# Kernel optimization log

Measured on AMD Instinct MI355X. Metric: run time of the kernel, lower is better.

The kernel has to match this reference:

```python
import jax, jax.numpy as jnp
import numpy as np

B, S, NX, H = 8, 1024, 1024, 16
D = NX // H  # head dim = 64


def setup_inputs() -> dict:
    key = jax.random.key(0)
    k1, k2, k3 = jax.random.split(key, 3)
    x = jax.random.normal(k1, (B, S, NX), dtype=jnp.float32)
    Wqkv = jax.random.normal(k2, (NX, 3 * NX), dtype=jnp.float32) * 0.02
    bqkv = jnp.zeros((3 * NX,), dtype=jnp.float32)
    Wproj = jax.random.normal(k3, (NX, NX), dtype=jnp.float32) * 0.02
    bproj = jnp.zeros((NX,), dtype=jnp.float32)
    return {"x": x, "Wqkv": Wqkv, "bqkv": bqkv, "Wproj": Wproj, "bproj": bproj}


def reference(x, Wqkv, bqkv, Wproj, bproj):
    # c_attn: Conv1D == x @ W + b
    qkv = jnp.einsum('bsn,nm->bsm', x, Wqkv) + bqkv  # [B,S,3*NX]
    q, k, v = jnp.split(qkv, 3, axis=-1)
    # split heads -> [B,H,S,D]
    def split_heads(t):
        return t.reshape(B, S, H, D).transpose(0, 2, 1, 3)
    q, k, v = split_heads(q), split_heads(k), split_heads(v)
    # present = stack(key, value) with key as [B,H,S,D]
    present = jnp.stack((k, v))  # [2,B,H,S,D]
    # scores, scaled (scale=True) by sqrt(head_dim)
    w = jnp.einsum('bhqd,bhkd->bhqk', q, k) / jnp.sqrt(jnp.asarray(D, x.dtype))
    bias = jnp.tril(jnp.ones((S, S), dtype=x.dtype))[None, None]  # causal tril buffer
    w = w * bias - 10000.0 * (1.0 - bias)
    w = jax.nn.softmax(w, axis=-1)
    a = jnp.einsum('bhqk,bhkd->bhqd', w, v)  # [B,H,S,D]
    a = a.transpose(0, 2, 1, 3).reshape(B, S, NX)  # merge heads
    a = jnp.einsum('bsn,nm->bsm', a, Wproj) + bproj  # c_proj
    return a, present
```

## Files before the change

### kernel.cpp

```cpp
#include <hip/hip_runtime.h>
#include <stdint.h>


#define BB 8
#define SS 1024
#define NXX 1024
#define NH 16
#define HD 64

typedef __bf16 bf16x8 __attribute__((ext_vector_type(8)));
typedef float  floatx4 __attribute__((ext_vector_type(4)));
typedef unsigned short ushort8 __attribute__((ext_vector_type(8)));
typedef unsigned short ushortx4 __attribute__((ext_vector_type(4)));

__device__ inline float bf2f(unsigned short u) {
    unsigned int x = ((unsigned int)u) << 16;
    float f;
    __builtin_memcpy(&f, &x, 4);
    return f;
}
__device__ inline unsigned short f2bf(float f) {
    unsigned int u;
    __builtin_memcpy(&u, &f, 4);
    u += 0x7FFFu + ((u >> 16) & 1u);
    return (unsigned short)(u >> 16);
}

__device__ inline void gload_lds16(const unsigned short* g, unsigned short* l) {
    __builtin_amdgcn_global_load_lds(
        (const __attribute__((address_space(1))) void*)g,
        (__attribute__((address_space(3))) void*)l, 16, 0, 0);
}

__global__ void sniff_k(const unsigned short* __restrict__ x, int* __restrict__ flag) {
    if (threadIdx.x == 0 && blockIdx.x == 0) {
        int g = 0;
        for (int i = 0; i < 512; i++) {
            float f = bf2f(x[i]);
            float a = fabsf(f);
            if (!(a <= 1e4f)) g++;
            else if (f != 0.f && a < 1e-35f) g++;
        }
        *flag = (g > 16) ? 1 : 0;
    }
}

__global__ __launch_bounds__(256) void prep(
    const void* __restrict__ x, const void* __restrict__ Wqkv,
    const void* __restrict__ Wproj,
    unsigned short* __restrict__ xbf, unsigned short* __restrict__ WqkvT,
    unsigned short* __restrict__ WprojT, const int* __restrict__ flagp) {
    const int f32 = *flagp;
    int blk = blockIdx.x;
    if (blk < 4096) {
        const size_t i = ((size_t)blk * 256 + threadIdx.x) * 8;
        if (f32) {
            const floatx4* p = (const floatx4*)((const float*)x + i);
            floatx4 f0 = p[0], f1 = p[1];
            ushort8 u;
#pragma unroll
            for (int j = 0; j < 4; j++) { u[j] = f2bf(f0[j]); u[4 + j] = f2bf(f1[j]); }
            *(ushort8*)(xbf + i) = u;
        } else {
            *(ushort8*)(xbf + i) = *(const ushort8*)((const unsigned short*)x + i);
        }
        return;
    }
    blk -= 4096;
    const void* in;
    unsigned short* out;
    int R, C;
    if (blk < 3072) { in = Wqkv; out = WqkvT; R = 1024; C = 3072; }
    else            { blk -= 3072; in = Wproj; out = WprojT; R = 1024; C = 1024; }
    const int ctiles = C / 32;
    const int c0 = (blk % ctiles) * 32, r0 = (blk / ctiles) * 32;

    __shared__ unsigned short tile[32][33];
    const int tx = threadIdx.x & 31, ty = threadIdx.x >> 5;
    if (f32) {
        const float* inf = (const float*)in;
#pragma unroll
        for (int i = ty; i < 32; i += 8)
            tile[i][tx] = f2bf(inf[(size_t)(r0 + i) * C + c0 + tx]);
    } else {
        const unsigned short* inu = (const unsigned short*)in;
#pragma unroll
        for (int i = ty; i < 32; i += 8)
            tile[i][tx] = inu[(size_t)(r0 + i) * C + c0 + tx];
    }
    __syncthreads();
#pragma unroll
    for (int i = ty; i < 32; i += 8)
        out[(size_t)(c0 + i) * R + r0 + tx] = tile[tx][i];
}

__global__ __launch_bounds__(256) void transpose_v(
    const void* __restrict__ outbase, unsigned short* __restrict__ vbfT,
    const int* __restrict__ flagp) {
    const int f32 = *flagp;
    const int blk = blockIdx.x;
    const int sb = blk & 15;
    const int bh = blk >> 4;
    const int tid = threadIdx.x;
    const int r = tid >> 2;
    const int c0 = (tid & 3) * 16;
    __shared__ unsigned short tile[64][72];
    const int perm = ((r & 15) << 2) | (r >> 4);
    const size_t esz = f32 ? 4 : 2;
    const char* vbase = (const char*)outbase + (size_t)(2 * BB * SS * NXX) * esz;
    if (f32) {
        const float* src = (const float*)vbase + ((size_t)bh * SS + sb * 64 + r) * HD + c0;
#pragma unroll
        for (int j = 0; j < 16; j++) tile[c0 + j][perm] = f2bf(src[j]);
    } else {
        const unsigned short* src = (const unsigned short*)vbase + ((size_t)bh * SS + sb * 64 + r) * HD + c0;
#pragma unroll
        for (int j = 0; j < 16; j++) tile[c0 + j][perm] = src[j];
    }
    __syncthreads();
    const int d = tid >> 2;
    const int o0 = (tid & 3) * 16;
    unsigned short* dst = vbfT + ((size_t)(bh * HD + d)) * SS + sb * 64 + o0;
    *(ushort8*)dst       = *(const ushort8*)&tile[d][o0];
    *(ushort8*)(dst + 8) = *(const ushort8*)&tile[d][o0 + 8];
}

template <int MODE>
__global__ __launch_bounds__(256) void gemm_bt(
    const unsigned short* __restrict__ A,
    const unsigned short* __restrict__ Bt,
    const void* __restrict__ bias,
    void* __restrict__ outbase,
    unsigned short* __restrict__ q_ws,
    unsigned short* __restrict__ kbf,
    int M, int N, int K, const int* __restrict__ flagp) {
    __shared__ __align__(16) unsigned short As[128 * 32];
    __shared__ __align__(16) unsigned short Bs[128 * 32];

    const int f32 = *flagp;
    const int tid  = threadIdx.x;
    const int lane = tid & 63;
    const int wave = tid >> 6;
    const int wr = wave >> 1, wc = wave & 1;
    const int l15 = lane & 15;
    const int quad = lane >> 4;
    const int row0 = blockIdx.y * 128;
    const int col0 = blockIdx.x * 128;

    floatx4 acc[4][4];
    floatx4 zz = {0.f, 0.f, 0.f, 0.f};
#pragma unroll
    for (int i = 0; i < 4; i++)
#pragma unroll
        for (int j = 0; j < 4; j++) acc[i][j] = zz;

    const int lrow = lane >> 2;
    const int lcol = (lane & 3) * 8;
    const unsigned short* Ag = A  + (size_t)(row0 + wave * 32 + lrow) * K + lcol;
    const unsigned short* Bg = Bt + (size_t)(col0 + wave * 32 + lrow) * K + lcol;
    unsigned short* Asl0 = &As[(wave * 32) * 32];
    unsigned short* Asl1 = &As[(wave * 32 + 16) * 32];
    unsigned short* Bsl0 = &Bs[(wave * 32) * 32];
    unsigned short* Bsl1 = &Bs[(wave * 32 + 16) * 32];

    for (int k0 = 0; k0 < K; k0 += 32) {
        gload_lds16(Ag + k0, Asl0);
        gload_lds16(Ag + k0 + (size_t)16 * K, Asl1);
        gload_lds16(Bg + k0, Bsl0);
        gload_lds16(Bg + k0 + (size_t)16 * K, Bsl1);
        __syncthreads();

        bf16x8 af[4], bfr[4];
#pragma unroll
        for (int mi = 0; mi < 4; mi++)
            af[mi] = *(const bf16x8*)&As[(wr * 64 + mi * 16 + l15) * 32 + quad * 8];
#pragma unroll
        for (int ni = 0; ni < 4; ni++)
            bfr[ni] = *(const bf16x8*)&Bs[(wc * 64 + ni * 16 + l15) * 32 + quad * 8];
#pragma unroll
        for (int mi = 0; mi < 4; mi++)
#pragma unroll
            for (int ni = 0; ni < 4; ni++)
                acc[mi][ni] = __builtin_amdgcn_mfma_f32_16x16x32_bf16(af[mi], bfr[ni], acc[mi][ni], 0, 0, 0);
        __syncthreads();
    }

    float bv[4];
#pragma unroll
    for (int ni = 0; ni < 4; ni++) {
        const int colb = col0 + wc * 64 + ni * 16 + l15;
        bv[ni] = f32 ? ((const float*)bias)[colb] : bf2f(((const unsigned short*)bias)[colb]);
    }

    if (MODE == 0) {
#pragma unroll
        for (int mi = 0; mi < 4; mi++)
#pragma unroll
            for (int ni = 0; ni < 4; ni++) {
                const int colb = col0 + wc * 64 + ni * 16 + l15;
#pragma unroll
                for (int i = 0; i < 4; i++) {
                    const int row = row0 + wr * 64 + mi * 16 + quad * 4 + i;
                    const float val = acc[mi][ni][i] + bv[ni];
                    const size_t idx = (size_t)row * N + colb;
                    if (f32) ((float*)outbase)[idx] = val;
                    else     ((unsigned short*)outbase)[idx] = f2bf(val);
                }
            }
        return;
    }

    const int sec = col0 >> 10;
    const size_t esz = f32 ? 4 : 2;
    const int b = row0 >> 10;
    const int s0 = row0 & 1023;

    if (sec == 0) {
#pragma unroll
        for (int mi = 0; mi < 4; mi++)
#pragma unroll
            for (int ni = 0; ni < 4; ni++) {
                const int colb = col0 + wc * 64 + ni * 16 + l15;
                const int h = (colb & 1023) >> 6, d = colb & 63;
#pragma unroll
                for (int i = 0; i < 4; i++) {
                    const int s = s0 + wr * 64 + mi * 16 + quad * 4 + i;
                    q_ws[(size_t)((b * NH + h) * SS + s) * HD + d] = f2bf(acc[mi][ni][i] + bv[ni]);
                }
            }
    } else if (sec == 1) {
        char* kbase = (char*)outbase + (size_t)(BB * SS * NXX) * esz;
#pragma unroll
        for (int mi = 0; mi < 4; mi++)
#pragma unroll
            for (int ni = 0; ni < 4; ni++) {
                const int colb = col0 + wc * 64 + ni * 16 + l15;
                const int h = (colb & 1023) >> 6, d = colb & 63;
#pragma unroll
                for (int i = 0; i < 4; i++) {
                    const int s = s0 + wr * 64 + mi * 16 + quad * 4 + i;
                    const float val = acc[mi][ni][i] + bv[ni];
                    const size_t idx = (size_t)((b * NH + h) * SS + s) * HD + d;
                    if (f32) ((float*)kbase)[idx] = val;
                    else     ((unsigned short*)kbase)[idx] = f2bf(val);
                    kbf[idx] = f2bf(val);
                }
            }
    } else {
        char* vbase = (char*)outbase + (size_t)(2 * BB * SS * NXX) * esz;
#pragma unroll
        for (int mi = 0; mi < 4; mi++)
#pragma unroll
            for (int ni = 0; ni < 4; ni++) {
                const int colb = col0 + wc * 64 + ni * 16 + l15;
                const int h = (colb & 1023) >> 6, d = colb & 63;
#pragma unroll
                for (int i = 0; i < 4; i++) {
                    const int s = s0 + wr * 64 + mi * 16 + quad * 4 + i;
                    const float val = acc[mi][ni][i] + bv[ni];
                    const size_t idx = (size_t)((b * NH + h) * SS + s) * HD + d;
                    if (f32) ((float*)vbase)[idx] = val;
                    else     ((unsigned short*)vbase)[idx] = f2bf(val);
                }
            }
    }
}

__global__ __launch_bounds__(256) void attn(
    const unsigned short* __restrict__ q_ws,
    const unsigned short* __restrict__ kbf,
    const unsigned short* __restrict__ vbfT,
    unsigned short* __restrict__ amerged) {
    const int tid = threadIdx.x;
    const int lane = tid & 63;
    const int w = tid >> 6;
    const int l15 = lane & 15, quad = lane >> 4;
    const int blk = blockIdx.x;
    const int p = blk & 3;
    const int bh = blk >> 2;
    const int b = bh >> 4, h = bh & 15;

    const unsigned short* Q = q_ws + (size_t)bh * (SS * HD);
    const unsigned short* K = kbf + (size_t)bh * (SS * HD);
    const unsigned short* V = vbfT + (size_t)bh * (HD * SS);

    __shared__ __align__(16) unsigned short Ks[64][72];
    __shared__ __align__(16) unsigned short Vs[64][72];
    __shared__ __align__(16) unsigned short Pl[4][32][72];

    floatx4 zz = {0.f, 0.f, 0.f, 0.f};
    ushort8 ones_u;
#pragma unroll
    for (int j = 0; j < 8; j++) ones_u[j] = 0x3F80;
    const bf16x8 ones = __builtin_bit_cast(bf16x8, ones_u);

    const int srow = tid >> 2;
    const int soff = (tid & 3) * 16;

#pragma unroll
    for (int tile = 0; tile < 2; tile++) {
        const int qb = tile ? (7 - p) : p;
        const int qbase = qb * 128;
        const int wrow0 = qbase + w * 32;
        const int wq_max = wrow0 + 31;
        const int jend = qbase + 128;

        bf16x8 qa[2][2];
#pragma unroll
        for (int m = 0; m < 2; m++)
#pragma unroll
            for (int t = 0; t < 2; t++)
                qa[m][t] = *(const bf16x8*)&Q[(size_t)(wrow0 + m * 16 + l15) * HD + t * 32 + quad * 8];

        floatx4 o[2][4], o5[2];
        float mrow[2][4];
#pragma unroll
        for (int m = 0; m < 2; m++) {
            o5[m] = zz;
#pragma unroll
            for (int i = 0; i < 4; i++) mrow[m][i] = -1e30f;
#pragma unroll
            for (int nf = 0; nf < 4; nf++) o[m][nf] = zz;
        }

        *(ushort8*)&Ks[srow][soff]     = *(const ushort8*)&K[(size_t)srow * HD + soff];
        *(ushort8*)&Ks[srow][soff + 8] = *(const ushort8*)&K[(size_t)srow * HD + soff + 8];
        *(ushort8*)&Vs[srow][soff]     = *(const ushort8*)&V[(size_t)srow * SS + soff];
        *(ushort8*)&Vs[srow][soff + 8] = *(const ushort8*)&V[(size_t)srow * SS + soff + 8];
        __syncthreads();

        for (int j0 = 0; j0 < jend; j0 += 64) {
            const bool havenext = (j0 + 64 < jend);
            ushort8 kn0, kn1, vn0, vn1;
            if (havenext) {
                kn0 = *(const ushort8*)&K[(size_t)(j0 + 64 + srow) * HD + soff];
                kn1 = *(const ushort8*)&K[(size_t)(j0 + 64 + srow) * HD + soff + 8];
                vn0 = *(const ushort8*)&V[(size_t)srow * SS + j0 + 64 + soff];
                vn1 = *(const ushort8*)&V[(size_t)srow * SS + j0 + 64 + soff + 8];
            }

            if (j0 <= wq_max) {
                floatx4 sf[2][4];
#pragma unroll
                for (int kg = 0; kg < 4; kg++) {
                    bf16x8 kb0 = *(const bf16x8*)&Ks[kg * 16 + l15][quad * 8];
                    bf16x8 kb1 = *(const bf16x8*)&Ks[kg * 16 + l15][32 + quad * 8];
#pragma unroll
                    for (int m = 0; m < 2; m++) {
                        floatx4 s = zz;
                        s = __builtin_amdgcn_mfma_f32_16x16x32_bf16(qa[m][0], kb0, s, 0, 0, 0);
                        s = __builtin_amdgcn_mfma_f32_16x16x32_bf16(qa[m][1], kb1, s, 0, 0, 0);
                        sf[m][kg] = s;
                    }
                }

                float alpha_[2][4];
#pragma unroll
                for (int m = 0; m < 2; m++)
#pragma unroll
                    for (int i = 0; i < 4; i++) {
                        const int qrow = wrow0 + m * 16 + quad * 4 + i;
                        float pv4[4];
#pragma unroll
                        for (int kg = 0; kg < 4; kg++) {
                            const int key = j0 + kg * 16 + l15;
                            float s = sf[m][kg][i] * 0.125f;
                            if (key > qrow) s = -10000.0f;
                            pv4[kg] = s;
                        }
                        float t = fmaxf(fmaxf(pv4[0], pv4[1]), fmaxf(pv4[2], pv4[3]));
                        t = fmaxf(t, __shfl_xor(t, 1));
                        t = fmaxf(t, __shfl_xor(t, 2));
                        t = fmaxf(t, __shfl_xor(t, 4));
                        t = fmaxf(t, __shfl_xor(t, 8));
                        const float mnew = fmaxf(mrow[m][i], t);
                        alpha_[m][i] = __expf(mrow[m][i] - mnew);
                        mrow[m][i] = mnew;
                        ushortx4 pk;
#pragma unroll
                        for (int kg = 0; kg < 4; kg++)
                            pk[kg] = f2bf(__expf(pv4[kg] - mnew));
                        *(ushortx4*)&Pl[w][m * 16 + quad * 4 + i][l15 * 4] = pk;
                    }

#pragma unroll
                for (int m = 0; m < 2; m++) {
#pragma unroll
                    for (int i = 0; i < 4; i++) o5[m][i] *= alpha_[m][i];
#pragma unroll
                    for (int nf = 0; nf < 4; nf++)
#pragma unroll
                        for (int i = 0; i < 4; i++) o[m][nf][i] *= alpha_[m][i];
                }

                bf16x8 pa[2][2];
#pragma unroll
                for (int m = 0; m < 2; m++) {
                    pa[m][0] = *(const bf16x8*)&Pl[w][m * 16 + l15][quad * 8];
                    pa[m][1] = *(const bf16x8*)&Pl[w][m * 16 + l15][32 + quad * 8];
                }

#pragma unroll
                for (int m = 0; m < 2; m++) {
                    o5[m] = __builtin_amdgcn_mfma_f32_16x16x32_bf16(pa[m][0], ones, o5[m], 0, 0, 0);
                    o5[m] = __builtin_amdgcn_mfma_f32_16x16x32_bf16(pa[m][1], ones, o5[m], 0, 0, 0);
                }
#pragma unroll
                for (int nf = 0; nf < 4; nf++) {
                    bf16x8 vb0 = *(const bf16x8*)&Vs[nf * 16 + l15][quad * 8];
                    bf16x8 vb1 = *(const bf16x8*)&Vs[nf * 16 + l15][32 + quad * 8];
#pragma unroll
                    for (int m = 0; m < 2; m++) {
                        o[m][nf] = __builtin_amdgcn_mfma_f32_16x16x32_bf16(pa[m][0], vb0, o[m][nf], 0, 0, 0);
                        o[m][nf] = __builtin_amdgcn_mfma_f32_16x16x32_bf16(pa[m][1], vb1, o[m][nf], 0, 0, 0);
                    }
                }
            }
            __syncthreads();
            if (havenext) {
                *(ushort8*)&Ks[srow][soff]     = kn0;
                *(ushort8*)&Ks[srow][soff + 8] = kn1;
                *(ushort8*)&Vs[srow][soff]     = vn0;
                *(ushort8*)&Vs[srow][soff + 8] = vn1;
            }
            __syncthreads();
        }

#pragma unroll
        for (int m = 0; m < 2; m++)
#pragma unroll
            for (int nf = 0; nf < 4; nf++)
#pragma unroll
                for (int i = 0; i < 4; i++) {
                    const int s = wrow0 + m * 16 + quad * 4 + i;
                    amerged[(size_t)(b * SS + s) * NXX + h * HD + nf * 16 + l15] =
                        f2bf(o[m][nf][i] / o5[m][i]);
                }
        __syncthreads();
    }
}

extern "C" void kernel_launch(void* const* d_in, const int* in_sizes, int n_in,
                              void* d_out, int out_size, void* d_ws, size_t ws_size,
                              hipStream_t stream) {
    const void* x     = d_in[0];
    const void* Wqkv  = d_in[1];
    const void* bqkv  = d_in[2];
    const void* Wproj = d_in[3];
    const void* bproj = d_in[4];

    int* flag = (int*)d_ws;
    unsigned short* ws = (unsigned short*)d_ws + 8;
    unsigned short* WqkvT   = ws;
    unsigned short* WprojT  = WqkvT + 3072 * 1024;
    unsigned short* q_ws    = WprojT + 1024 * 1024;
    unsigned short* kbf     = q_ws + 8 * 1024 * 1024;
    unsigned short* vbfT    = kbf + 8 * 1024 * 1024;
    unsigned short* amerged = vbfT + 8 * 1024 * 1024;
    unsigned short* xbf     = amerged;

    sniff_k<<<1, 64, 0, stream>>>((const unsigned short*)x, flag);
    prep<<<dim3(8192), 256, 0, stream>>>(x, Wqkv, Wproj, xbf, WqkvT, WprojT, flag);
    gemm_bt<1><<<dim3(3072 / 128, 8192 / 128), 256, 0, stream>>>(
        xbf, WqkvT, bqkv, d_out, q_ws, kbf, 8192, 3072, 1024, flag);
    transpose_v<<<dim3(128 * 16), 256, 0, stream>>>(d_out, vbfT, flag);
    attn<<<dim3(BB * NH * 4), 256, 0, stream>>>(q_ws, kbf, vbfT, amerged);
    gemm_bt<0><<<dim3(1024 / 128, 8192 / 128), 256, 0, stream>>>(
        amerged, WprojT, bproj, d_out, nullptr, nullptr, 8192, 1024, 1024, flag);
}
```

Before: 374.7 us.

## Double-buffer GEMM LDS tiles and read attention K/V directly from global

The GEMM kernel now double-buffers its A/B shared-memory tiles and issues the next tile's global-to-LDS loads before computing on the current one, so each k-step needs one barrier instead of two. The attention kernel drops the shared K/V staging and its block-wide barriers. Each wave now loads its K and V fragments straight from global memory and runs only up to its own causal limit. This removes sync stalls and lets waves proceed independently, at the cost of redundant per-wave global/L2 reads of K and V. It also relies on an explicit lgkmcnt wait to order the per-wave P-tile writes before they are read back.

New measurement: 390.6 us. 4.3% more time.

```diff
diff --git a/kernel.cpp b/kernel.cpp
--- a/kernel.cpp
+++ b/kernel.cpp
@@ -134,8 +134,8 @@
     unsigned short* __restrict__ q_ws,
     unsigned short* __restrict__ kbf,
     int M, int N, int K, const int* __restrict__ flagp) {
-    __shared__ __align__(16) unsigned short As[128 * 32];
-    __shared__ __align__(16) unsigned short Bs[128 * 32];
+    __shared__ __align__(16) unsigned short As[2][128 * 32];
+    __shared__ __align__(16) unsigned short Bs[2][128 * 32];
 
     const int f32 = *flagp;
     const int tid  = threadIdx.x;
@@ -158,31 +158,41 @@
     const int lcol = (lane & 3) * 8;
     const unsigned short* Ag = A  + (size_t)(row0 + wave * 32 + lrow) * K + lcol;
     const unsigned short* Bg = Bt + (size_t)(col0 + wave * 32 + lrow) * K + lcol;
-    unsigned short* Asl0 = &As[(wave * 32) * 32];
-    unsigned short* Asl1 = &As[(wave * 32 + 16) * 32];
-    unsigned short* Bsl0 = &Bs[(wave * 32) * 32];
-    unsigned short* Bsl1 = &Bs[(wave * 32 + 16) * 32];
-
+    const int sl0 = (wave * 32) * 32;
+    const int sl1 = (wave * 32 + 16) * 32;
+
+    gload_lds16(Ag, &As[0][sl0]);
+    gload_lds16(Ag + (size_t)16 * K, &As[0][sl1]);
+    gload_lds16(Bg, &Bs[0][sl0]);
+    gload_lds16(Bg + (size_t)16 * K, &Bs[0][sl1]);
+    __syncthreads();
+
+    int cur = 0;
     for (int k0 = 0; k0 < K; k0 += 32) {
-        gload_lds16(Ag + k0, Asl0);
-        gload_lds16(Ag + k0 + (size_t)16 * K, Asl1);
-        gload_lds16(Bg + k0, Bsl0);
-        gload_lds16(Bg + k0 + (size_t)16 * K, Bsl1);
-        __syncthreads();
+        if (k0 + 32 < K) {
+            const unsigned short* Agn = Ag + k0 + 32;
+            const unsigned short* Bgn = Bg + k0 + 32;
+            gload_lds16(Agn, &As[cur ^ 1][sl0]);
+            gload_lds16(Agn + (size_t)16 * K, &As[cur ^ 1][sl1]);
+            gload_lds16(Bgn, &Bs[cur ^ 1][sl0]);
+            gload_lds16(Bgn + (size_t)16 * K, &Bs[cur ^ 1][sl1]);
+        }
 
         bf16x8 af[4], bfr[4];
 #pragma unroll
         for (int mi = 0; mi < 4; mi++)
-            af[mi] = *(const bf16x8*)&As[(wr * 64 + mi * 16 + l15) * 32 + quad * 8];
+            af[mi] = *(const bf16x8*)&As[cur][(wr * 64 + mi * 16 + l15) * 32 + quad * 8];
 #pragma unroll
         for (int ni = 0; ni < 4; ni++)
-            bfr[ni] = *(const bf16x8*)&Bs[(wc * 64 + ni * 16 + l15) * 32 + quad * 8];
+            bfr[ni] = *(const bf16x8*)&Bs[cur][(wc * 64 + ni * 16 + l15) * 32 + quad * 8];
 #pragma unroll
         for (int mi = 0; mi < 4; mi++)
 #pragma unroll
             for (int ni = 0; ni < 4; ni++)
                 acc[mi][ni] = __builtin_amdgcn_mfma_f32_16x16x32_bf16(af[mi], bfr[ni], acc[mi][ni], 0, 0, 0);
+
         __syncthreads();
+        cur ^= 1;
     }
 
     float bv[4];
@@ -284,8 +294,6 @@
     const unsigned short* K = kbf + (size_t)bh * (SS * HD);
     const unsigned short* V = vbfT + (size_t)bh * (HD * SS);
 
-    __shared__ __align__(16) unsigned short Ks[64][72];
-    __shared__ __align__(16) unsigned short Vs[64][72];
     __shared__ __align__(16) unsigned short Pl[4][32][72];
 
     floatx4 zz = {0.f, 0.f, 0.f, 0.f};
@@ -294,16 +302,11 @@
     for (int j = 0; j < 8; j++) ones_u[j] = 0x3F80;
     const bf16x8 ones = __builtin_bit_cast(bf16x8, ones_u);
 
-    const int srow = tid >> 2;
-    const int soff = (tid & 3) * 16;
-
 #pragma unroll
     for (int tile = 0; tile < 2; tile++) {
         const int qb = tile ? (7 - p) : p;
-        const int qbase = qb * 128;
-        const int wrow0 = qbase + w * 32;
+        const int wrow0 = qb * 128 + w * 32;
         const int wq_max = wrow0 + 31;
-        const int jend = qbase + 128;
 
         bf16x8 qa[2][2];
 #pragma unroll
@@ -323,107 +326,87 @@
             for (int nf = 0; nf < 4; nf++) o[m][nf] = zz;
         }
 
-        *(ushort8*)&Ks[srow][soff]     = *(const ushort8*)&K[(size_t)srow * HD + soff];
-        *(ushort8*)&Ks[srow][soff + 8] = *(const ushort8*)&K[(size_t)srow * HD + soff + 8];
-        *(ushort8*)&Vs[srow][soff]     = *(const ushort8*)&V[(size_t)srow * SS + soff];
-        *(ushort8*)&Vs[srow][soff + 8] = *(const ushort8*)&V[(size_t)srow * SS + soff + 8];
-        __syncthreads();
-
-        for (int j0 = 0; j0 < jend; j0 += 64) {
-            const bool havenext = (j0 + 64 < jend);
-            ushort8 kn0, kn1, vn0, vn1;
-            if (havenext) {
-                kn0 = *(const ushort8*)&K[(size_t)(j0 + 64 + srow) * HD + soff];
-                kn1 = *(const ushort8*)&K[(size_t)(j0 + 64 + srow) * HD + soff + 8];
-                vn0 = *(const ushort8*)&V[(size_t)srow * SS + j0 + 64 + soff];
-                vn1 = *(const ushort8*)&V[(size_t)srow * SS + j0 + 64 + soff + 8];
-            }
-
-            if (j0 <= wq_max) {
-                floatx4 sf[2][4];
-#pragma unroll
-                for (int kg = 0; kg < 4; kg++) {
-                    bf16x8 kb0 = *(const bf16x8*)&Ks[kg * 16 + l15][quad * 8];
-                    bf16x8 kb1 = *(const bf16x8*)&Ks[kg * 16 + l15][32 + quad * 8];
-#pragma unroll
-                    for (int m = 0; m < 2; m++) {
-                        floatx4 s = zz;
-                        s = __builtin_amdgcn_mfma_f32_16x16x32_bf16(qa[m][0], kb0, s, 0, 0, 0);
-                        s = __builtin_amdgcn_mfma_f32_16x16x32_bf16(qa[m][1], kb1, s, 0, 0, 0);
-                        sf[m][kg] = s;
+        for (int j0 = 0; j0 <= wq_max; j0 += 64) {
+            floatx4 sf[2][4];
+#pragma unroll
+            for (int kg = 0; kg < 4; kg++) {
+                const size_t krow = (size_t)(j0 + kg * 16 + l15) * HD;
+                bf16x8 kb0 = *(const bf16x8*)&K[krow + quad * 8];
+                bf16x8 kb1 = *(const bf16x8*)&K[krow + 32 + quad * 8];
+#pragma unroll
+                for (int m = 0; m < 2; m++) {
+                    floatx4 s = zz;
+                    s = __builtin_amdgcn_mfma_f32_16x16x32_bf16(qa[m][0], kb0, s, 0, 0, 0);
+                    s = __builtin_amdgcn_mfma_f32_16x16x32_bf16(qa[m][1], kb1, s, 0, 0, 0);
+                    sf[m][kg] = s;
+                }
+            }
+
+            float alpha_[2][4];
+#pragma unroll
+            for (int m = 0; m < 2; m++)
+#pragma unroll
+                for (int i = 0; i < 4; i++) {
+                    const int qrow = wrow0 + m * 16 + quad * 4 + i;
+                    float pv4[4];
+#pragma unroll
+                    for (int kg = 0; kg < 4; kg++) {
+                        const int key = j0 + kg * 16 + l15;
+                        float s = sf[m][kg][i] * 0.125f;
+                        if (key > qrow) s = -10000.0f;
+                        pv4[kg] = s;
                     }
-                }
-
-                float alpha_[2][4];
-#pragma unroll
-                for (int m = 0; m < 2; m++)
-#pragma unroll
-                    for (int i = 0; i < 4; i++) {
-                        const int qrow = wrow0 + m * 16 + quad * 4 + i;
-                        float pv4[4];
-#pragma unroll
-                        for (int kg = 0; kg < 4; kg++) {
-                            const int key = j0 + kg * 16 + l15;
-                            float s = sf[m][kg][i] * 0.125f;
-                            if (key > qrow) s = -10000.0f;
-                            pv4[kg] = s;
-                        }
-                        float t = fmaxf(fmaxf(pv4[0], pv4[1]), fmaxf(pv4[2], pv4[3]));
-                        t = fmaxf(t, __shfl_xor(t, 1));
-                        t = fmaxf(t, __shfl_xor(t, 2));
-                        t = fmaxf(t, __shfl_xor(t, 4));
-                        t = fmaxf(t, __shfl_xor(t, 8));
-                        const float mnew = fmaxf(mrow[m][i], t);
-                        alpha_[m][i] = __expf(mrow[m][i] - mnew);
-                        mrow[m][i] = mnew;
-                        ushortx4 pk;
-#pragma unroll
-                        for (int kg = 0; kg < 4; kg++)
-                            pk[kg] = f2bf(__expf(pv4[kg] - mnew));
-                        *(ushortx4*)&Pl[w][m * 16 + quad * 4 + i][l15 * 4] = pk;
-                    }
-
+                    float t = fmaxf(fmaxf(pv4[0], pv4[1]), fmaxf(pv4[2], pv4[3]));
+                    t = fmaxf(t, __shfl_xor(t, 1));
+                    t = fmaxf(t, __shfl_xor(t, 2));
+                    t = fmaxf(t, __shfl_xor(t, 4));
+                    t = fmaxf(t, __shfl_xor(t, 8));
+                    const float mnew = fmaxf(mrow[m][i], t);
+                    alpha_[m][i] = __expf(mrow[m][i] - mnew);
+                    mrow[m][i] = mnew;
+                    ushortx4 pk;
+#pragma unroll
+                    for (int kg = 0; kg < 4; kg++)
+                        pk[kg] = f2bf(__expf(pv4[kg] - mnew));
+                    *(ushortx4*)&Pl[w][m * 16 + quad * 4 + i][l15 * 4] = pk;
+                }
+
+#pragma unroll
+            for (int m = 0; m < 2; m++) {
+#pragma unroll
+                for (int i = 0; i < 4; i++) o5[m][i] *= alpha_[m][i];
+#pragma unroll
+                for (int nf = 0; nf < 4; nf++)
+#pragma unroll
+                    for (int i = 0; i < 4; i++) o[m][nf][i] *= alpha_[m][i];
+            }
+
+            asm volatile("s_waitcnt lgkmcnt(0)" ::: "memory");
+            __builtin_amdgcn_sched_barrier(0);
+
+            bf16x8 pa[2][2];
+#pragma unroll
+            for (int m = 0; m < 2; m++) {
+                pa[m][0] = *(const bf16x8*)&Pl[w][m * 16 + l15][quad * 8];
+                pa[m][1] = *(const bf16x8*)&Pl[w][m * 16 + l15][32 + quad * 8];
+            }
+
+#pragma unroll
+            for (int m = 0; m < 2; m++) {
+                o5[m] = __builtin_amdgcn_mfma_f32_16x16x32_bf16(pa[m][0], ones, o5[m], 0, 0, 0);
+                o5[m] = __builtin_amdgcn_mfma_f32_16x16x32_bf16(pa[m][1], ones, o5[m], 0, 0, 0);
+            }
+#pragma unroll
+            for (int nf = 0; nf < 4; nf++) {
+                const size_t vrow = (size_t)(nf * 16 + l15) * SS + j0;
+                bf16x8 vb0 = *(const bf16x8*)&V[vrow + quad * 8];
+                bf16x8 vb1 = *(const bf16x8*)&V[vrow + 32 + quad * 8];
 #pragma unroll
                 for (int m = 0; m < 2; m++) {
-#pragma unroll
-                    for (int i = 0; i < 4; i++) o5[m][i] *= alpha_[m][i];
-#pragma unroll
-                    for (int nf = 0; nf < 4; nf++)
-#pragma unroll
-                        for (int i = 0; i < 4; i++) o[m][nf][i] *= alpha_[m][i];
-                }
-
-                bf16x8 pa[2][2];
-#pragma unroll
-                for (int m = 0; m < 2; m++) {
-                    pa[m][0] = *(const bf16x8*)&Pl[w][m * 16 + l15][quad * 8];
-                    pa[m][1] = *(const bf16x8*)&Pl[w][m * 16 + l15][32 + quad * 8];
-                }
-
-#pragma unroll
-                for (int m = 0; m < 2; m++) {
-                    o5[m] = __builtin_amdgcn_mfma_f32_16x16x32_bf16(pa[m][0], ones, o5[m], 0, 0, 0);
-                    o5[m] = __builtin_amdgcn_mfma_f32_16x16x32_bf16(pa[m][1], ones, o5[m], 0, 0, 0);
-                }
-#pragma unroll
-                for (int nf = 0; nf < 4; nf++) {
-                    bf16x8 vb0 = *(const bf16x8*)&Vs[nf * 16 + l15][quad * 8];
-                    bf16x8 vb1 = *(const bf16x8*)&Vs[nf * 16 + l15][32 + quad * 8];
-#pragma unroll
-                    for (int m = 0; m < 2; m++) {
-                        o[m][nf] = __builtin_amdgcn_mfma_f32_16x16x32_bf16(pa[m][0], vb0, o[m][nf], 0, 0, 0);
-                        o[m][nf] = __builtin_amdgcn_mfma_f32_16x16x32_bf16(pa[m][1], vb1, o[m][nf], 0, 0, 0);
-                    }
-                }
-            }
-            __syncthreads();
-            if (havenext) {
-                *(ushort8*)&Ks[srow][soff]     = kn0;
-                *(ushort8*)&Ks[srow][soff + 8] = kn1;
-                *(ushort8*)&Vs[srow][soff]     = vn0;
-                *(ushort8*)&Vs[srow][soff + 8] = vn1;
-            }
-            __syncthreads();
+                    o[m][nf] = __builtin_amdgcn_mfma_f32_16x16x32_bf16(pa[m][0], vb0, o[m][nf], 0, 0, 0);
+                    o[m][nf] = __builtin_amdgcn_mfma_f32_16x16x32_bf16(pa[m][1], vb1, o[m][nf], 0, 0, 0);
+                }
+            }
         }
 
 #pragma unroll
@@ -436,7 +419,6 @@
                     amerged[(size_t)(b * SS + s) * NXX + h * HD + nf * 16 + l15] =
                         f2bf(o[m][nf][i] / o5[m][i]);
                 }
-        __syncthreads();
     }
 }
 
```

## Rewrite GEMMs as 256x256-tile 8-wave kernels with double-buffered pipelined loads

Applied to the files above, without the earlier changes.

Replaces the 128x128, 4-wave GEMM with a 256x256-tile, 8-wave kernel. It double-buffers A and B in LDS with XOR-swizzled layout and K-step 64, and issues the next tiles' global-to-LDS loads in phases between MFMA bursts, using raw barriers, vmcnt waits and setprio. Block IDs are remapped to group tiles for locality. The aim is to hide global load latency, raise data reuse per tile and cut LDS bank conflicts. In exchange it needs far more registers and LDS (128KB) and leaves fewer blocks, e.g. 128 for the projection GEMM, which may underfill the 256 CUs.

Measured after the change: 346.7 us. -7.4%, faster.

```diff
diff --git a/kernel.cpp b/kernel.cpp
--- a/kernel.cpp
+++ b/kernel.cpp
@@ -7,6 +7,8 @@
 #define NXX 1024
 #define NH 16
 #define HD 64
+#define KK 1024
+#define NKT 16
 
 typedef __bf16 bf16x8 __attribute__((ext_vector_type(8)));
 typedef float  floatx4 __attribute__((ext_vector_type(4)));
@@ -31,6 +33,16 @@
         (const __attribute__((address_space(1))) void*)g,
         (__attribute__((address_space(3))) void*)l, 16, 0, 0);
 }
+
+__device__ inline void barrier_raw() {
+    asm volatile("" ::: "memory");
+    __builtin_amdgcn_sched_barrier(0);
+    __builtin_amdgcn_s_barrier();
+    __builtin_amdgcn_sched_barrier(0);
+    asm volatile("" ::: "memory");
+}
+#define WAIT_VM4() asm volatile("s_waitcnt vmcnt(4)" ::: "memory")
+#define WAIT_VM0() asm volatile("s_waitcnt vmcnt(0)" ::: "memory")
 
 __global__ void sniff_k(const unsigned short* __restrict__ x, int* __restrict__ flag) {
     if (threadIdx.x == 0 && blockIdx.x == 0) {
@@ -125,83 +137,123 @@
     *(ushort8*)(dst + 8) = *(const ushort8*)&tile[d][o0 + 8];
 }
 
+#define STAGE_A(slot, h, kt) do { \
+    const unsigned short* sg_ = Ab + (size_t)((h) * 128) * KK + (size_t)(kt) * 64; \
+    gload_lds16(sg_, &As[slot][h][w * 512]); \
+    gload_lds16(sg_ + (size_t)64 * KK, &As[slot][h][4096 + w * 512]); \
+} while (0)
+#define STAGE_B(slot, h, kt) do { \
+    const unsigned short* sg_ = Bb + (size_t)((h) * 128) * KK + (size_t)(kt) * 64; \
+    gload_lds16(sg_, &Bs[slot][h][w * 512]); \
+    gload_lds16(sg_ + (size_t)64 * KK, &Bs[slot][h][4096 + w * 512]); \
+} while (0)
+#define PHASE(qq, STAGE_STMT, TAIL) do { \
+    bf16x8 a_[2][2]; \
+    _Pragma("unroll") \
+    for (int mm = 0; mm < 2; mm++) { \
+        const int arow = (qq) * 32 + mm * 16 + l15; \
+        a_[mm][0] = *(const bf16x8*)&Ah[arow * 64 + fo0]; \
+        a_[mm][1] = *(const bf16x8*)&Ah[arow * 64 + fo1]; \
+    } \
+    STAGE_STMT; \
+    barrier_raw(); \
+    __builtin_amdgcn_s_setprio(1); \
+    _Pragma("unroll") \
+    for (int mm = 0; mm < 2; mm++) \
+    _Pragma("unroll") \
+    for (int nf = 0; nf < 4; nf++) { \
+        acc[2 * (qq) + mm][nf] = __builtin_amdgcn_mfma_f32_16x16x32_bf16(a_[mm][0], bfr[nf][0], acc[2 * (qq) + mm][nf], 0, 0, 0); \
+        acc[2 * (qq) + mm][nf] = __builtin_amdgcn_mfma_f32_16x16x32_bf16(a_[mm][1], bfr[nf][1], acc[2 * (qq) + mm][nf], 0, 0, 0); \
+    } \
+    __builtin_amdgcn_s_setprio(0); \
+    TAIL; \
+    barrier_raw(); \
+} while (0)
+
 template <int MODE>
-__global__ __launch_bounds__(256) void gemm_bt(
+__global__ __launch_bounds__(512, 2) void gemm8p(
     const unsigned short* __restrict__ A,
     const unsigned short* __restrict__ Bt,
     const void* __restrict__ bias,
     void* __restrict__ outbase,
     unsigned short* __restrict__ q_ws,
     unsigned short* __restrict__ kbf,
-    int M, int N, int K, const int* __restrict__ flagp) {
-    __shared__ __align__(16) unsigned short As[128 * 32];
-    __shared__ __align__(16) unsigned short Bs[128 * 32];
+    int M, int N, int Nt, const int* __restrict__ flagp) {
+    __shared__ __align__(16) unsigned short As[2][2][128 * 64];
+    __shared__ __align__(16) unsigned short Bs[2][2][128 * 64];
 
     const int f32 = *flagp;
     const int tid  = threadIdx.x;
     const int lane = tid & 63;
-    const int wave = tid >> 6;
-    const int wr = wave >> 1, wc = wave & 1;
+    const int w = tid >> 6;
+    const int r = w >> 2;
+    const int c = w & 3;
+    const int bh2 = c >> 1;
     const int l15 = lane & 15;
     const int quad = lane >> 4;
-    const int row0 = blockIdx.y * 128;
-    const int col0 = blockIdx.x * 128;
-
-    floatx4 acc[4][4];
+
+    const int cpx = gridDim.x >> 3;
+    const int bid = (blockIdx.x & 7) * cpx + (blockIdx.x >> 3);
+    const int bx = bid % Nt, by = bid / Nt;
+    const int row0 = by * 256, col0 = bx * 256;
+
+    floatx4 acc[8][4];
     floatx4 zz = {0.f, 0.f, 0.f, 0.f};
 #pragma unroll
-    for (int i = 0; i < 4; i++)
+    for (int i = 0; i < 8; i++)
 #pragma unroll
         for (int j = 0; j < 4; j++) acc[i][j] = zz;
 
-    const int lrow = lane >> 2;
-    const int lcol = (lane & 3) * 8;
-    const unsigned short* Ag = A  + (size_t)(row0 + wave * 32 + lrow) * K + lcol;
-    const unsigned short* Bg = Bt + (size_t)(col0 + wave * 32 + lrow) * K + lcol;
-    unsigned short* Asl0 = &As[(wave * 32) * 32];
-    unsigned short* Asl1 = &As[(wave * 32 + 16) * 32];
-    unsigned short* Bsl0 = &Bs[(wave * 32) * 32];
-    unsigned short* Bsl1 = &Bs[(wave * 32 + 16) * 32];
-
-    for (int k0 = 0; k0 < K; k0 += 32) {
-        gload_lds16(Ag + k0, Asl0);
-        gload_lds16(Ag + k0 + (size_t)16 * K, Asl1);
-        gload_lds16(Bg + k0, Bsl0);
-        gload_lds16(Bg + k0 + (size_t)16 * K, Bsl1);
-        __syncthreads();
-
-        bf16x8 af[4], bfr[4];
-#pragma unroll
-        for (int mi = 0; mi < 4; mi++)
-            af[mi] = *(const bf16x8*)&As[(wr * 64 + mi * 16 + l15) * 32 + quad * 8];
-#pragma unroll
-        for (int ni = 0; ni < 4; ni++)
-            bfr[ni] = *(const bf16x8*)&Bs[(wc * 64 + ni * 16 + l15) * 32 + quad * 8];
-#pragma unroll
-        for (int mi = 0; mi < 4; mi++)
-#pragma unroll
-            for (int ni = 0; ni < 4; ni++)
-                acc[mi][ni] = __builtin_amdgcn_mfma_f32_16x16x32_bf16(af[mi], bfr[ni], acc[mi][ni], 0, 0, 0);
-        __syncthreads();
+    const int srow = tid >> 3;
+    const int scole = ((tid & 7) ^ (srow & 7)) << 3;
+    const unsigned short* Ab = A  + (size_t)(row0 + srow) * KK + scole;
+    const unsigned short* Bb = Bt + (size_t)(col0 + srow) * KK + scole;
+
+    const int fo0 = (quad << 3) ^ ((l15 & 7) << 3);
+    const int fo1 = fo0 ^ 32;
+
+    STAGE_A(0, 0, 0); STAGE_A(0, 1, 0);
+    STAGE_B(0, 0, 0); STAGE_B(0, 1, 0);
+    STAGE_B(1, 0, 1); STAGE_B(1, 1, 1);
+    WAIT_VM4();
+    barrier_raw();
+
+    bf16x8 bfr[4][2];
+#pragma unroll 2
+    for (int t = 0; t < NKT; t++) {
+        const int slot = t & 1;
+        const unsigned short* Ah = &As[slot][r][0];
+        const unsigned short* Bh = &Bs[slot][bh2][0];
+#pragma unroll
+        for (int nf = 0; nf < 4; nf++) {
+            const int brow = (c & 1) * 64 + nf * 16 + l15;
+            bfr[nf][0] = *(const bf16x8*)&Bh[brow * 64 + fo0];
+            bfr[nf][1] = *(const bf16x8*)&Bh[brow * 64 + fo1];
+        }
+        PHASE(0, { if (t + 1 < NKT) STAGE_A((t + 1) & 1, 0, t + 1); }, {});
+        PHASE(1, { if (t + 1 < NKT) STAGE_A((t + 1) & 1, 1, t + 1); }, {});
+        PHASE(2, { if (t + 2 < NKT) STAGE_B(slot, 0, t + 2); }, {});
+        PHASE(3, { if (t + 2 < NKT) STAGE_B(slot, 1, t + 2); },
+              { if (t < NKT - 2) { WAIT_VM4(); } else { WAIT_VM0(); } });
     }
 
     float bv[4];
 #pragma unroll
-    for (int ni = 0; ni < 4; ni++) {
-        const int colb = col0 + wc * 64 + ni * 16 + l15;
-        bv[ni] = f32 ? ((const float*)bias)[colb] : bf2f(((const unsigned short*)bias)[colb]);
+    for (int nf = 0; nf < 4; nf++) {
+        const int colb = col0 + c * 64 + nf * 16 + l15;
+        bv[nf] = f32 ? ((const float*)bias)[colb] : bf2f(((const unsigned short*)bias)[colb]);
     }
 
     if (MODE == 0) {
 #pragma unroll
-        for (int mi = 0; mi < 4; mi++)
-#pragma unroll
-            for (int ni = 0; ni < 4; ni++) {
-                const int colb = col0 + wc * 64 + ni * 16 + l15;
+        for (int mi = 0; mi < 8; mi++)
+#pragma unroll
+            for (int nf = 0; nf < 4; nf++) {
+                const int colb = col0 + c * 64 + nf * 16 + l15;
 #pragma unroll
                 for (int i = 0; i < 4; i++) {
-                    const int row = row0 + wr * 64 + mi * 16 + quad * 4 + i;
-                    const float val = acc[mi][ni][i] + bv[ni];
+                    const int row = row0 + r * 128 + mi * 16 + quad * 4 + i;
+                    const float val = acc[mi][nf][i] + bv[nf];
                     const size_t idx = (size_t)row * N + colb;
                     if (f32) ((float*)outbase)[idx] = val;
                     else     ((unsigned short*)outbase)[idx] = f2bf(val);
@@ -217,29 +269,29 @@
 
     if (sec == 0) {
 #pragma unroll
-        for (int mi = 0; mi < 4; mi++)
-#pragma unroll
-            for (int ni = 0; ni < 4; ni++) {
-                const int colb = col0 + wc * 64 + ni * 16 + l15;
+        for (int mi = 0; mi < 8; mi++)
+#pragma unroll
+            for (int nf = 0; nf < 4; nf++) {
+                const int colb = col0 + c * 64 + nf * 16 + l15;
                 const int h = (colb & 1023) >> 6, d = colb & 63;
 #pragma unroll
                 for (int i = 0; i < 4; i++) {
-                    const int s = s0 + wr * 64 + mi * 16 + quad * 4 + i;
-                    q_ws[(size_t)((b * NH + h) * SS + s) * HD + d] = f2bf(acc[mi][ni][i] + bv[ni]);
+                    const int s = s0 + r * 128 + mi * 16 + quad * 4 + i;
+                    q_ws[(size_t)((b * NH + h) * SS + s) * HD + d] = f2bf(acc[mi][nf][i] + bv[nf]);
                 }
             }
     } else if (sec == 1) {
         char* kbase = (char*)outbase + (size_t)(BB * SS * NXX) * esz;
 #pragma unroll
-        for (int mi = 0; mi < 4; mi++)
-#pragma unroll
-            for (int ni = 0; ni < 4; ni++) {
-                const int colb = col0 + wc * 64 + ni * 16 + l15;
+        for (int mi = 0; mi < 8; mi++)
+#pragma unroll
+            for (int nf = 0; nf < 4; nf++) {
+                const int colb = col0 + c * 64 + nf * 16 + l15;
                 const int h = (colb & 1023) >> 6, d = colb & 63;
 #pragma unroll
                 for (int i = 0; i < 4; i++) {
-                    const int s = s0 + wr * 64 + mi * 16 + quad * 4 + i;
-                    const float val = acc[mi][ni][i] + bv[ni];
+                    const int s = s0 + r * 128 + mi * 16 + quad * 4 + i;
+                    const float val = acc[mi][nf][i] + bv[nf];
                     const size_t idx = (size_t)((b * NH + h) * SS + s) * HD + d;
                     if (f32) ((float*)kbase)[idx] = val;
                     else     ((unsigned short*)kbase)[idx] = f2bf(val);
@@ -249,15 +301,15 @@
     } else {
         char* vbase = (char*)outbase + (size_t)(2 * BB * SS * NXX) * esz;
 #pragma unroll
-        for (int mi = 0; mi < 4; mi++)
-#pragma unroll
-            for (int ni = 0; ni < 4; ni++) {
-                const int colb = col0 + wc * 64 + ni * 16 + l15;
+        for (int mi = 0; mi < 8; mi++)
+#pragma unroll
+            for (int nf = 0; nf < 4; nf++) {
+                const int colb = col0 + c * 64 + nf * 16 + l15;
                 const int h = (colb & 1023) >> 6, d = colb & 63;
 #pragma unroll
                 for (int i = 0; i < 4; i++) {
-                    const int s = s0 + wr * 64 + mi * 16 + quad * 4 + i;
-                    const float val = acc[mi][ni][i] + bv[ni];
+                    const int s = s0 + r * 128 + mi * 16 + quad * 4 + i;
+                    const float val = acc[mi][nf][i] + bv[nf];
                     const size_t idx = (size_t)((b * NH + h) * SS + s) * HD + d;
                     if (f32) ((float*)vbase)[idx] = val;
                     else     ((unsigned short*)vbase)[idx] = f2bf(val);
@@ -461,10 +513,10 @@
 
     sniff_k<<<1, 64, 0, stream>>>((const unsigned short*)x, flag);
     prep<<<dim3(8192), 256, 0, stream>>>(x, Wqkv, Wproj, xbf, WqkvT, WprojT, flag);
-    gemm_bt<1><<<dim3(3072 / 128, 8192 / 128), 256, 0, stream>>>(
-        xbf, WqkvT, bqkv, d_out, q_ws, kbf, 8192, 3072, 1024, flag);
+    gemm8p<1><<<dim3(12 * 32), 512, 0, stream>>>(
+        xbf, WqkvT, bqkv, d_out, q_ws, kbf, 8192, 3072, 12, flag);
     transpose_v<<<dim3(128 * 16), 256, 0, stream>>>(d_out, vbfT, flag);
     attn<<<dim3(BB * NH * 4), 256, 0, stream>>>(q_ws, kbf, vbfT, amerged);
-    gemm_bt<0><<<dim3(1024 / 128, 8192 / 128), 256, 0, stream>>>(
-        amerged, WprojT, bproj, d_out, nullptr, nullptr, 8192, 1024, 1024, flag);
-}
+    gemm8p<0><<<dim3(4 * 32), 512, 0, stream>>>(
+        amerged, WprojT, bproj, d_out, nullptr, nullptr, 8192, 1024, 4, flag);
+}
```
